# Optimization experiments

Hardware: AMD Instinct MI355X
Metric: run time of the kernel (lower is better)

## Reference

```python
import jax, jax.numpy as jnp
import numpy as np

# Adaptive softmax config (PyTorch AdaptiveLogSoftmaxWithLoss defaults, div_value=4)
N_CLASSES = 50000
CUTOFFS = (2000, 10000)          # shortlist size 2000; clusters [2000,10000), [10000,50000)
SHORTLIST = CUTOFFS[0]
HEAD_SIZE = SHORTLIST + 2        # shortlist + one logit per cluster
IN_FEAT = 512                    # output_size of MLP == in_features of adaptive softmax
HSZ0, HSZ1 = 128, 32             # in_features // 4**(i+1)
C0 = CUTOFFS[1] - CUTOFFS[0]     # 8000
C1 = N_CLASSES - CUTOFFS[1]      # 40000


def setup_inputs() -> dict:
    key = jax.random.key(0)
    ks = jax.random.split(key, 16)
    s = 0.02
    inp = {
        "x": jax.random.normal(ks[0], (4096, 512), jnp.float32),
        "t": jax.random.randint(ks[1], (4096,), 0, N_CLASSES, jnp.int64),
        # MLP params: 512 -> 2048 -> 128 -> 512, ReLU after each
        "W1": jax.random.normal(ks[2], (2048, 512), jnp.float32) * s,
        "b1": jnp.zeros((2048,), jnp.float32),
        "W2": jax.random.normal(ks[3], (128, 2048), jnp.float32) * s,
        "b2": jnp.zeros((128,), jnp.float32),
        "W3": jax.random.normal(ks[4], (512, 128), jnp.float32) * s,
        "b3": jnp.zeros((512,), jnp.float32),
        # adaptive softmax head: shortlist + 2 cluster logits
        "head_W": jax.random.normal(ks[5], (HEAD_SIZE, IN_FEAT), jnp.float32) * s,
        "head_b": jnp.zeros((HEAD_SIZE,), jnp.float32),
        # tail cluster 0: 512 -> 128 -> 8000 (no bias, no activation)
        "t0a": jax.random.normal(ks[6], (HSZ0, IN_FEAT), jnp.float32) * s,
        "t0b": jax.random.normal(ks[7], (C0, HSZ0), jnp.float32) * s,
        # tail cluster 1: 512 -> 32 -> 40000
        "t1a": jax.random.normal(ks[8], (HSZ1, IN_FEAT), jnp.float32) * s,
        "t1b": jax.random.normal(ks[9], (C1, HSZ1), jnp.float32) * s,
    }
    return inp


def _mlp(x, W1, b1, W2, b2, W3, b3):
    h = jax.nn.relu(x @ W1.T + b1)
    h = jax.nn.relu(h @ W2.T + b2)
    return jax.nn.relu(h @ W3.T + b3)   # [N, 512]


def _adaptive_log_softmax(score, t, head_W, head_b, t0a, t0b, t1a, t1b):
    n = score.shape[0]
    rows = jnp.arange(n)
    head_lsm = jax.nn.log_softmax(score @ head_W.T + head_b, axis=-1)   # [N, 2002]
    # tail clusters: two low-rank projections then log-softmax over cluster classes
    tail0_lsm = jax.nn.log_softmax((score @ t0a.T) @ t0b.T, axis=-1)    # [N, 8000]
    tail1_lsm = jax.nn.log_softmax((score @ t1a.T) @ t1b.T, axis=-1)    # [N, 40000]

    lp_short = head_lsm[rows, jnp.clip(t, 0, SHORTLIST - 1)]
    lp_c0 = head_lsm[:, SHORTLIST] + tail0_lsm[rows, jnp.clip(t - CUTOFFS[0], 0, C0 - 1)]
    lp_c1 = head_lsm[:, SHORTLIST + 1] + tail1_lsm[rows, jnp.clip(t - CUTOFFS[1], 0, C1 - 1)]

    out = jnp.where(t < CUTOFFS[0], lp_short, jnp.where(t < CUTOFFS[1], lp_c0, lp_c1))  # [N]
    loss = -jnp.mean(out)
    return out, loss


def reference(x, t, W1, b1, W2, b2, W3, b3, head_W, head_b, t0a, t0b, t1a, t1b):
    score = _mlp(x, W1, b1, W2, b2, W3, b3)
    out, loss = _adaptive_log_softmax(score, t, head_W, head_b, t0a, t0b, t1a, t1b)
    return out, loss
```

## Files before the change

### kernel.cpp

```cpp
#include <hip/hip_runtime.h>
#include <math.h>

typedef __attribute__((ext_vector_type(8))) short bf16x8;
typedef __attribute__((ext_vector_type(4))) float f32x4;

#define NROWS 4096
#define SHORTLIST 2000
#define HEADC 2002
#define CUT1 10000
#define C0_CLS 8000
#define C1_CLS 40000
#define L2E 1.4426950408889634f
#define LN2 0.6931471805599453f

#define NH_P  16
#define NC0_P 25
#define NC1_P 125

__device__ __forceinline__ float fexp2(float x) {
#if __has_builtin(__builtin_amdgcn_exp2f)
  return __builtin_amdgcn_exp2f(x);
#else
  return exp2f(x);
#endif
}

__device__ __forceinline__ unsigned short f2b(float f) {
  unsigned u = __float_as_uint(f);
  unsigned r = (u + 0x7FFFu + ((u >> 16) & 1u)) >> 16;
  return (unsigned short)r;
}
__device__ __forceinline__ float b2f(unsigned short u) {
  return __uint_as_float(((unsigned)u) << 16);
}

__device__ __forceinline__ void xcd_swz(int& bx, int& by) {
  const int gx = gridDim.x;
  const int nwg = gx * gridDim.y;
  const int orig = by * gx + bx;
  const int wg = (orig & 7) * (nwg >> 3) + (orig >> 3);
  bx = wg % gx;
  by = wg / gx;
}

__global__ __launch_bounds__(256) void cvt_all(
    const float* __restrict__ s0, unsigned short* __restrict__ d0,
    const float* __restrict__ s1, unsigned short* __restrict__ d1,
    const float* __restrict__ s2, unsigned short* __restrict__ d2,
    const float* __restrict__ s3, unsigned short* __restrict__ d3,
    const float* __restrict__ s4, unsigned short* __restrict__ d4,
    const float* __restrict__ s5, unsigned short* __restrict__ d5,
    const float* __restrict__ s6, unsigned short* __restrict__ d6,
    const float* __restrict__ s7, unsigned short* __restrict__ d7,
    const float* __restrict__ s8, unsigned short* __restrict__ d8)
{
  const float* src; unsigned short* dst; int n4;
  switch (blockIdx.y) {
    case 0: src = s0; dst = d0; n4 = 4096 * 512 / 4;   break;
    case 1: src = s1; dst = d1; n4 = 2048 * 512 / 4;   break;
    case 2: src = s2; dst = d2; n4 = 128 * 2048 / 4;   break;
    case 3: src = s3; dst = d3; n4 = 512 * 128 / 4;    break;
    case 4: src = s4; dst = d4; n4 = HEADC * 512 / 4;  break;
    case 5: src = s5; dst = d5; n4 = 128 * 512 / 4;    break;
    case 6: src = s6; dst = d6; n4 = 8000 * 128 / 4;   break;
    case 7: src = s7; dst = d7; n4 = 32 * 512 / 4;     break;
    default: src = s8; dst = d8; n4 = 40000 * 32 / 4;  break;
  }
  for (int i = blockIdx.x * 256 + threadIdx.x; i < n4; i += 256 * gridDim.x) {
    float4 v = ((const float4*)src)[i];
    ushort4 o;
    o.x = f2b(v.x); o.y = f2b(v.y); o.z = f2b(v.z); o.w = f2b(v.w);
    ((ushort4*)dst)[i] = o;
  }
}

template<bool BIAS, bool RELU, bool F32OUT, bool SCL>
__global__ __launch_bounds__(256) void gemm_lds(
    const unsigned short* __restrict__ A, const unsigned short* __restrict__ W,
    const float* __restrict__ bias, void* __restrict__ outp,
    int M, int N, int lda, int Kseg)
{
  __shared__ __align__(16) unsigned short As[128 * 32];
  __shared__ __align__(16) unsigned short Bs[128 * 32];

  int bx = blockIdx.x, by = blockIdx.y;
  xcd_swz(bx, by);

  const int tid  = threadIdx.x;
  const int lane = tid & 63;
  const int wv   = tid >> 6;
  const int cl   = lane & 15;
  const int ko   = lane >> 4;
  const int wr   = (wv >> 1) * 64;
  const int wc   = (wv & 1) * 64;
  const int row0 = by * 128;
  const int col0 = bx * 128;
  const int koff = blockIdx.z * Kseg;

  const int sr0 = tid >> 2;
  const int ssl = tid & 3;

  f32x4 acc[4][4];
#pragma unroll
  for (int p = 0; p < 4; ++p)
#pragma unroll
    for (int q = 0; q < 4; ++q) acc[p][q] = (f32x4){0.f, 0.f, 0.f, 0.f};

  const unsigned short* aSrc = A + (size_t)(row0 + sr0) * lda + koff + ssl * 8;
  const unsigned short* bSrc = W + (size_t)(col0 + sr0) * lda + koff + ssl * 8;
  const size_t half = (size_t)64 * lda;

  bf16x8 sa0 = *(const bf16x8*)(aSrc);
  bf16x8 sa1 = *(const bf16x8*)(aSrc + half);
  bf16x8 sb0 = *(const bf16x8*)(bSrc);
  bf16x8 sb1 = *(const bf16x8*)(bSrc + half);

  const int nK = Kseg / 32;
  for (int ks = 0; ks < nK; ++ks) {
    __syncthreads();
    *(bf16x8*)&As[(size_t)sr0 * 32 + ssl * 8]        = sa0;
    *(bf16x8*)&As[(size_t)(sr0 + 64) * 32 + ssl * 8] = sa1;
    *(bf16x8*)&Bs[(size_t)sr0 * 32 + ssl * 8]        = sb0;
    *(bf16x8*)&Bs[(size_t)(sr0 + 64) * 32 + ssl * 8] = sb1;
    __syncthreads();
    if (ks + 1 < nK) {
      const int k1 = (ks + 1) * 32;
      sa0 = *(const bf16x8*)(aSrc + k1);
      sa1 = *(const bf16x8*)(aSrc + k1 + half);
      sb0 = *(const bf16x8*)(bSrc + k1);
      sb1 = *(const bf16x8*)(bSrc + k1 + half);
    }
    bf16x8 aF[4], bF[4];
#pragma unroll
    for (int p = 0; p < 4; ++p)
      aF[p] = *(const bf16x8*)&As[(size_t)(wr + p * 16 + cl) * 32 + ko * 8];
#pragma unroll
    for (int q = 0; q < 4; ++q)
      bF[q] = *(const bf16x8*)&Bs[(size_t)(wc + q * 16 + cl) * 32 + ko * 8];
#pragma unroll
    for (int p = 0; p < 4; ++p)
#pragma unroll
      for (int q = 0; q < 4; ++q)
        acc[p][q] = __builtin_amdgcn_mfma_f32_16x16x32_bf16(aF[p], bF[q], acc[p][q], 0, 0, 0);
  }

  if constexpr (F32OUT) {
    float* P = (float*)outp + (size_t)blockIdx.z * M * N;
#pragma unroll
    for (int q = 0; q < 4; ++q) {
      const int col = col0 + wc + q * 16 + cl;
#pragma unroll
      for (int p = 0; p < 4; ++p)
#pragma unroll
        for (int j = 0; j < 4; ++j) {
          const int R = row0 + wr + p * 16 + 4 * ko + j;
          P[(size_t)R * N + col] = acc[p][q][j];
        }
    }
  } else {
    unsigned short* C = (unsigned short*)outp;
#pragma unroll
    for (int q = 0; q < 4; ++q) {
      const int col = col0 + wc + q * 16 + cl;
      float bs = 0.f;
      if (BIAS) bs = bias[col];
#pragma unroll
      for (int p = 0; p < 4; ++p)
#pragma unroll
        for (int j = 0; j < 4; ++j) {
          const int R = row0 + wr + p * 16 + 4 * ko + j;
          float v = acc[p][q][j] + bs;
          if (RELU) v = fmaxf(v, 0.f);
          if (SCL)  v *= L2E;
          C[(size_t)R * N + col] = f2b(v);
        }
    }
  }
}

template<int SK, bool BIAS, bool RELU>
__global__ __launch_bounds__(256) void splitk_reduce(
    const float* __restrict__ P, const float* __restrict__ bias,
    unsigned short* __restrict__ out, int MN4, int N)
{
  const int i = blockIdx.x * 256 + threadIdx.x;
  if (i >= MN4) return;
  float4 v = ((const float4*)P)[i];
#pragma unroll
  for (int z = 1; z < SK; ++z) {
    float4 p = ((const float4*)(P + (size_t)z * MN4 * 4))[i];
    v.x += p.x; v.y += p.y; v.z += p.z; v.w += p.w;
  }
  if (BIAS) {
    const int col = (i % (N / 4)) * 4;
    float4 b = *(const float4*)(bias + col);
    v.x += b.x; v.y += b.y; v.z += b.z; v.w += b.w;
  }
  if (RELU) {
    v.x = fmaxf(v.x, 0.f); v.y = fmaxf(v.y, 0.f);
    v.z = fmaxf(v.z, 0.f); v.w = fmaxf(v.w, 0.f);
  }
  ushort4 o;
  o.x = f2b(v.x); o.y = f2b(v.y); o.z = f2b(v.z); o.w = f2b(v.w);
  ((ushort4*)out)[i] = o;
}

__global__ __launch_bounds__(256) void head_gemm_lse(
    const unsigned short* __restrict__ A,
    const unsigned short* __restrict__ W,
    const float* __restrict__ bias,
    float* __restrict__ pm, float* __restrict__ ps)
{
  __shared__ __align__(16) unsigned short As[128 * 32];
  __shared__ __align__(16) unsigned short Bs[128 * 32];
  __shared__ float lm[4][64], ls[4][64];

  int bx = blockIdx.x, by = blockIdx.y;
  xcd_swz(bx, by);

  const int lda  = 512;
  const int tid  = threadIdx.x;
  const int lane = tid & 63;
  const int wv   = tid >> 6;
  const int cl   = lane & 15;
  const int ko   = lane >> 4;
  const int wr   = (wv >> 1) * 64;
  const int wc   = (wv & 1) * 64;
  const int row0 = by * 128;
  const int col0 = bx * 128;

  const int sr0 = tid >> 2;
  const int ssl = tid & 3;

  f32x4 acc[4][4];
#pragma unroll
  for (int p = 0; p < 4; ++p)
#pragma unroll
    for (int q = 0; q < 4; ++q) acc[p][q] = (f32x4){0.f, 0.f, 0.f, 0.f};

  const unsigned short* aSrc = A + (size_t)(row0 + sr0) * lda + ssl * 8;
  const unsigned short* bSrc0 = W + (size_t)min(col0 + sr0, HEADC - 1) * lda + ssl * 8;
  const unsigned short* bSrc1 = W + (size_t)min(col0 + sr0 + 64, HEADC - 1) * lda + ssl * 8;
  const size_t half = (size_t)64 * lda;

  bf16x8 sa0 = *(const bf16x8*)(aSrc);
  bf16x8 sa1 = *(const bf16x8*)(aSrc + half);
  bf16x8 sb0 = *(const bf16x8*)(bSrc0);
  bf16x8 sb1 = *(const bf16x8*)(bSrc1);

  const int nK = 512 / 32;
  for (int ks = 0; ks < nK; ++ks) {
    __syncthreads();
    *(bf16x8*)&As[(size_t)sr0 * 32 + ssl * 8]        = sa0;
    *(bf16x8*)&As[(size_t)(sr0 + 64) * 32 + ssl * 8] = sa1;
    *(bf16x8*)&Bs[(size_t)sr0 * 32 + ssl * 8]        = sb0;
    *(bf16x8*)&Bs[(size_t)(sr0 + 64) * 32 + ssl * 8] = sb1;
    __syncthreads();
    if (ks + 1 < nK) {
      const int k1 = (ks + 1) * 32;
      sa0 = *(const bf16x8*)(aSrc + k1);
      sa1 = *(const bf16x8*)(aSrc + k1 + half);
      sb0 = *(const bf16x8*)(bSrc0 + k1);
      sb1 = *(const bf16x8*)(bSrc1 + k1);
    }
    bf16x8 aF[4], bF[4];
#pragma unroll
    for (int p = 0; p < 4; ++p)
      aF[p] = *(const bf16x8*)&As[(size_t)(wr + p * 16 + cl) * 32 + ko * 8];
#pragma unroll
    for (int q = 0; q < 4; ++q)
      bF[q] = *(const bf16x8*)&Bs[(size_t)(wc + q * 16 + cl) * 32 + ko * 8];
#pragma unroll
    for (int p = 0; p < 4; ++p)
#pragma unroll
      for (int q = 0; q < 4; ++q)
        acc[p][q] = __builtin_amdgcn_mfma_f32_16x16x32_bf16(aF[p], bF[q], acc[p][q], 0, 0, 0);
  }

  float bl2[4]; int colq[4];
#pragma unroll
  for (int q = 0; q < 4; ++q) {
    colq[q] = col0 + wc + q * 16 + cl;
    bl2[q] = bias[min(colq[q], HEADC - 1)] * L2E;
  }

  float mr[4][4], sr_[4][4];
#pragma unroll
  for (int p = 0; p < 4; ++p)
#pragma unroll
    for (int j = 0; j < 4; ++j) {
      float vv[4];
#pragma unroll
      for (int q = 0; q < 4; ++q) {
        float v = acc[p][q][j] + bl2[q];
        if (colq[q] >= HEADC) v = -1e30f;
        vv[q] = v;
      }
      const float mm = fmaxf(fmaxf(vv[0], vv[1]), fmaxf(vv[2], vv[3]));
      float ss = 0.f;
#pragma unroll
      for (int q = 0; q < 4; ++q) ss += fexp2(vv[q] - mm);
      mr[p][j] = mm;
      sr_[p][j] = ss;
    }

#pragma unroll
  for (int mask = 1; mask <= 8; mask <<= 1) {
#pragma unroll
    for (int p = 0; p < 4; ++p)
#pragma unroll
      for (int j = 0; j < 4; ++j) {
        const float mo = __shfl_xor(mr[p][j], mask);
        const float so = __shfl_xor(sr_[p][j], mask);
        const float mn = fmaxf(mr[p][j], mo);
        sr_[p][j] = sr_[p][j] * fexp2(mr[p][j] - mn) + so * fexp2(mo - mn);
        mr[p][j] = mn;
      }
  }

  if (cl == 0) {
#pragma unroll
    for (int p = 0; p < 4; ++p)
#pragma unroll
      for (int j = 0; j < 4; ++j) {
        lm[wv][p * 16 + 4 * ko + j] = mr[p][j];
        ls[wv][p * 16 + 4 * ko + j] = sr_[p][j];
      }
  }
  __syncthreads();
  if (tid < 128) {
    const int pair = tid >> 6, idx = tid & 63;
    const float m0 = lm[pair * 2][idx], m1 = lm[pair * 2 + 1][idx];
    const float M = fmaxf(m0, m1);
    const float S = ls[pair * 2][idx] * fexp2(m0 - M) + ls[pair * 2 + 1][idx] * fexp2(m1 - M);
    const int grow = row0 + tid;
    pm[(size_t)bx * NROWS + grow] = M;
    ps[(size_t)bx * NROWS + grow] = S;
  }
}

template<int WR, int WC, bool BIAS, bool RELU>
__global__ __launch_bounds__(256) void gemm_mfma(
    const unsigned short* __restrict__ A, const unsigned short* __restrict__ W,
    const float* __restrict__ bias, unsigned short* __restrict__ C,
    int M, int N, int K)
{
  const int lane = threadIdx.x & 63;
  const int wv   = threadIdx.x >> 6;
  const int cl   = lane & 15;
  const int ko   = lane >> 4;
  const int rw   = (blockIdx.y * WR + (wv / WC)) * 64;
  const int cw   = (blockIdx.x * WC + (wv % WC)) * 32;

  f32x4 acc[4][2];
#pragma unroll
  for (int p = 0; p < 4; ++p)
#pragma unroll
    for (int q = 0; q < 2; ++q) acc[p][q] = (f32x4){0.f, 0.f, 0.f, 0.f};

  const unsigned short* ap = A + (size_t)(rw + cl) * K + ko * 8;
  const unsigned short* bp = W + (size_t)(cw + cl) * K + ko * 8;
  const size_t rstep = (size_t)16 * K;

#pragma unroll 2
  for (int kb = 0; kb < K; kb += 32) {
    bf16x8 a[4], b[2];
#pragma unroll
    for (int p = 0; p < 4; ++p) a[p] = *(const bf16x8*)(ap + p * rstep + kb);
#pragma unroll
    for (int q = 0; q < 2; ++q) b[q] = *(const bf16x8*)(bp + q * rstep + kb);
#pragma unroll
    for (int p = 0; p < 4; ++p)
#pragma unroll
      for (int q = 0; q < 2; ++q)
        acc[p][q] = __builtin_amdgcn_mfma_f32_16x16x32_bf16(a[p], b[q], acc[p][q], 0, 0, 0);
  }

#pragma unroll
  for (int q = 0; q < 2; ++q) {
    const int col = cw + q * 16 + cl;
    if (col >= N) continue;
    float bs = 0.f;
    if (BIAS) bs = bias[col];
#pragma unroll
    for (int p = 0; p < 4; ++p) {
#pragma unroll
      for (int j = 0; j < 4; ++j) {
        const int R = rw + p * 16 + 4 * ko + j;
        float v = acc[p][q][j] + bs;
        if (RELU) v = fmaxf(v, 0.f);
        C[(size_t)R * N + col] = f2b(v);
      }
    }
  }
}

template<int KBLK, int ROWT, int U, int NIT>
__global__ __launch_bounds__(256) void fused_lse_tail(
    const unsigned short* __restrict__ H,
    const unsigned short* __restrict__ W,
    int NCB,
    float* __restrict__ pm, float* __restrict__ ps)
{
  const int K    = KBLK * 32;
  const int lane = threadIdx.x & 63;
  const int wv   = threadIdx.x >> 6;
  const int cl   = lane & 15;
  const int ko   = lane >> 4;
  const int r0   = blockIdx.x * (64 * ROWT) + wv * (16 * ROWT);

  bf16x8 aF[ROWT][KBLK];
#pragma unroll
  for (int rt = 0; rt < ROWT; ++rt) {
    const unsigned short* ap = H + (size_t)(r0 + rt * 16 + cl) * K + ko * 8;
#pragma unroll
    for (int kk = 0; kk < KBLK; ++kk) aF[rt][kk] = *(const bf16x8*)(ap + kk * 32);
  }

  float m[ROWT][4], s[ROWT][4], s2[ROWT][4];
#pragma unroll
  for (int rt = 0; rt < ROWT; ++rt)
#pragma unroll
    for (int j = 0; j < 4; ++j) { m[rt][j] = -1e30f; s[rt][j] = 0.f; s2[rt][j] = 0.f; }

  const unsigned short* wbase =
      W + (size_t)(blockIdx.y * (U * NIT) * 16 + cl) * K + ko * 8;
  const size_t chunkstep = (size_t)16 * K;

  bf16x8 bA[U][KBLK], bB[U][KBLK];

  auto loadB = [&](bf16x8 (&bf)[U][KBLK], int it) {
    const unsigned short* p = wbase + (size_t)it * U * chunkstep;
#pragma unroll
    for (int u = 0; u < U; ++u)
#pragma unroll
      for (int kk = 0; kk < KBLK; ++kk)
        bf[u][kk] = *(const bf16x8*)(p + u * chunkstep + kk * 32);
  };

  auto consume = [&](bf16x8 (&bf)[U][KBLK]) {
    f32x4 acc[ROWT][U];
#pragma unroll
    for (int rt = 0; rt < ROWT; ++rt)
#pragma unroll
      for (int u = 0; u < U; ++u) acc[rt][u] = (f32x4){0.f, 0.f, 0.f, 0.f};
#pragma unroll
    for (int kk = 0; kk < KBLK; ++kk)
#pragma unroll
      for (int u = 0; u < U; ++u)
#pragma unroll
        for (int rt = 0; rt < ROWT; ++rt)
          acc[rt][u] = __builtin_amdgcn_mfma_f32_16x16x32_bf16(aF[rt][kk], bf[u][kk], acc[rt][u], 0, 0, 0);

    float cm[ROWT][4];
#pragma unroll
    for (int rt = 0; rt < ROWT; ++rt)
#pragma unroll
      for (int j = 0; j < 4; ++j) {
        float c = acc[rt][0][j];
#pragma unroll
        for (int u = 1; u < U; ++u) c = fmaxf(c, acc[rt][u][j]);
        cm[rt][j] = c;
      }

    float dd = -3e38f;
#pragma unroll
    for (int rt = 0; rt < ROWT; ++rt)
#pragma unroll
      for (int j = 0; j < 4; ++j) dd = fmaxf(dd, cm[rt][j] - m[rt][j]);

    if (__any(dd > 8.f)) {
#pragma unroll
      for (int rt = 0; rt < ROWT; ++rt)
#pragma unroll
        for (int j = 0; j < 4; ++j) {
          const float mn = fmaxf(m[rt][j], cm[rt][j]);
          const float sc = fexp2(m[rt][j] - mn);
          s[rt][j] *= sc; s2[rt][j] *= sc;
          m[rt][j] = mn;
        }
    }
#pragma unroll
    for (int rt = 0; rt < ROWT; ++rt)
#pragma unroll
      for (int u = 0; u < U; ++u)
#pragma unroll
        for (int j = 0; j < 4; ++j) {
          const float e = fexp2(acc[rt][u][j] - m[rt][j]);
          if (u & 1) s2[rt][j] += e; else s[rt][j] += e;
        }
  };

  loadB(bA, 0);
#pragma unroll
  for (int it = 0; it < NIT; it += 2) {
    loadB(bB, it + 1);
    consume(bA);
    if (it + 2 < NIT) loadB(bA, it + 2);
    consume(bB);
  }

#pragma unroll
  for (int rt = 0; rt < ROWT; ++rt)
#pragma unroll
    for (int j = 0; j < 4; ++j) s[rt][j] += s2[rt][j];

#pragma unroll
  for (int mask = 1; mask <= 8; mask <<= 1) {
#pragma unroll
    for (int rt = 0; rt < ROWT; ++rt)
#pragma unroll
      for (int j = 0; j < 4; ++j) {
        const float mo = __shfl_xor(m[rt][j], mask);
        const float so = __shfl_xor(s[rt][j], mask);
        const float mn = fmaxf(m[rt][j], mo);
        s[rt][j] = s[rt][j] * fexp2(m[rt][j] - mn) + so * fexp2(mo - mn);
        m[rt][j] = mn;
      }
  }
  if (cl == 0) {
#pragma unroll
    for (int rt = 0; rt < ROWT; ++rt)
#pragma unroll
      for (int j = 0; j < 4; ++j) {
        const int R = r0 + rt * 16 + 4 * ko + j;
        pm[(size_t)blockIdx.y * NROWS + R] = m[rt][j];
        ps[(size_t)blockIdx.y * NROWS + R] = s[rt][j];
      }
  }
}

__global__ __launch_bounds__(256) void gather_kernel(
    const unsigned short* __restrict__ Sb,
    const unsigned short* __restrict__ hWb,
    const float* __restrict__ head_b,
    const unsigned short* __restrict__ h0b,
    const unsigned short* __restrict__ t0bb,
    const unsigned short* __restrict__ h1b,
    const unsigned short* __restrict__ t1bb,
    const int* __restrict__ t,
    float* __restrict__ gsh, float* __restrict__ gc0, float* __restrict__ gc1,
    float* __restrict__ tg0, float* __restrict__ tg1)
{
  const int lane = threadIdx.x & 63;
  const int row  = blockIdx.x * 4 + (threadIdx.x >> 6);
  const int tv   = t[row];
  const int ch   = min(max(tv, 0), SHORTLIST - 1);
  const int c0   = min(max(tv - SHORTLIST, 0), C0_CLS - 1);
  const int c1   = min(max(tv - CUT1, 0), C1_CLS - 1);

  float acc[5] = {0.f, 0.f, 0.f, 0.f, 0.f};

  {
    bf16x8 sv = *(const bf16x8*)(Sb + (size_t)row * 512 + lane * 8);
    bf16x8 w0 = *(const bf16x8*)(hWb + (size_t)ch * 512 + lane * 8);
    bf16x8 w1 = *(const bf16x8*)(hWb + (size_t)SHORTLIST * 512 + lane * 8);
    bf16x8 w2 = *(const bf16x8*)(hWb + (size_t)(SHORTLIST + 1) * 512 + lane * 8);
#pragma unroll
    for (int e = 0; e < 8; ++e) {
      const float sf = b2f((unsigned short)sv[e]);
      acc[0] = fmaf(sf, b2f((unsigned short)w0[e]), acc[0]);
      acc[1] = fmaf(sf, b2f((unsigned short)w1[e]), acc[1]);
      acc[2] = fmaf(sf, b2f((unsigned short)w2[e]), acc[2]);
    }
  }
  if (lane < 16) {
    bf16x8 hv = *(const bf16x8*)(h0b + (size_t)row * 128 + lane * 8);
    bf16x8 wv = *(const bf16x8*)(t0bb + (size_t)c0 * 128 + lane * 8);
#pragma unroll
    for (int e = 0; e < 8; ++e)
      acc[3] = fmaf(b2f((unsigned short)hv[e]), b2f((unsigned short)wv[e]), acc[3]);
  }
  if (lane < 4) {
    bf16x8 hv = *(const bf16x8*)(h1b + (size_t)row * 32 + lane * 8);
    bf16x8 wv = *(const bf16x8*)(t1bb + (size_t)c1 * 32 + lane * 8);
#pragma unroll
    for (int e = 0; e < 8; ++e)
      acc[4] = fmaf(b2f((unsigned short)hv[e]), b2f((unsigned short)wv[e]), acc[4]);
  }

#pragma unroll
  for (int mask = 1; mask < 64; mask <<= 1)
#pragma unroll
    for (int k = 0; k < 5; ++k) acc[k] += __shfl_xor(acc[k], mask);

  if (lane == 0) {
    gsh[row] = acc[0] + head_b[ch] * L2E;
    gc0[row] = acc[1] + head_b[SHORTLIST] * L2E;
    gc1[row] = acc[2] + head_b[SHORTLIST + 1] * L2E;
    tg0[row] = acc[3];
    tg1[row] = acc[4];
  }
}

__global__ __launch_bounds__(256) void combine_kernel(
    const int* __restrict__ t,
    const float* __restrict__ pmh, const float* __restrict__ psh,
    const float* __restrict__ gsh, const float* __restrict__ gc0,
    const float* __restrict__ gc1,
    const float* __restrict__ pm0, const float* __restrict__ ps0,
    const float* __restrict__ tg0,
    const float* __restrict__ pm1, const float* __restrict__ ps1,
    const float* __restrict__ tg1,
    float* __restrict__ out)
{
  const int r = blockIdx.x * 256 + threadIdx.x;
  if (r >= NROWS) return;

  float M = -1e30f, S = 0.f;
  for (int c = 0; c < NH_P; ++c) M = fmaxf(M, pmh[c * NROWS + r]);
  for (int c = 0; c < NH_P; ++c) S += psh[c * NROWS + r] * fexp2(pmh[c * NROWS + r] - M);
  const float hl2 = M + log2f(S);

  const int tv = t[r];
  float o2;
  if (tv < SHORTLIST) {
    o2 = gsh[r] - hl2;
  } else if (tv < CUT1) {
    float M0 = -1e30f, S0 = 0.f;
    for (int c = 0; c < NC0_P; ++c) M0 = fmaxf(M0, pm0[c * NROWS + r]);
    for (int c = 0; c < NC0_P; ++c) S0 += ps0[c * NROWS + r] * fexp2(pm0[c * NROWS + r] - M0);
    o2 = (gc0[r] - hl2) + (tg0[r] - (M0 + log2f(S0)));
  } else {
    float M1 = -1e30f, S1 = 0.f;
    for (int c = 0; c < NC1_P; ++c) M1 = fmaxf(M1, pm1[c * NROWS + r]);
    for (int c = 0; c < NC1_P; ++c) S1 += ps1[c * NROWS + r] * fexp2(pm1[c * NROWS + r] - M1);
    o2 = (gc1[r] - hl2) + (tg1[r] - (M1 + log2f(S1)));
  }
  out[r] = o2 * LN2;
}

__global__ __launch_bounds__(256) void loss_kernel(
    const float* __restrict__ out, float* __restrict__ loss)
{
  __shared__ float sred[256];
  const int tid = threadIdx.x;
  float s = 0.f;
  for (int i = tid; i < NROWS; i += 256) s += out[i];
  sred[tid] = s;
  __syncthreads();
  for (int st = 128; st > 0; st >>= 1) {
    if (tid < st) sred[tid] += sred[tid + st];
    __syncthreads();
  }
  if (tid == 0) *loss = -sred[0] / (float)NROWS;
}

extern "C" void kernel_launch(void* const* d_in, const int* in_sizes, int n_in,
                              void* d_out, int out_size, void* d_ws, size_t ws_size,
                              hipStream_t stream)
{
  const float* x      = (const float*)d_in[0];
  const int*   t      = (const int*)  d_in[1];
  const float* W1     = (const float*)d_in[2];
  const float* b1     = (const float*)d_in[3];
  const float* W2     = (const float*)d_in[4];
  const float* b2     = (const float*)d_in[5];
  const float* W3     = (const float*)d_in[6];
  const float* b3     = (const float*)d_in[7];
  const float* head_W = (const float*)d_in[8];
  const float* head_b = (const float*)d_in[9];
  const float* t0a    = (const float*)d_in[10];
  const float* t0b    = (const float*)d_in[11];
  const float* t1a    = (const float*)d_in[12];
  const float* t1b    = (const float*)d_in[13];

  unsigned short* p16 = (unsigned short*)d_ws;
  unsigned short* xb  = p16; p16 += 4096ull * 512;
  unsigned short* W1b = p16; p16 += 2048ull * 512;
  unsigned short* W2b = p16; p16 += 128ull  * 2048;
  unsigned short* W3b = p16; p16 += 512ull  * 128;
  unsigned short* hWb = p16; p16 += (size_t)HEADC * 512;
  unsigned short* t0ab= p16; p16 += 128ull  * 512;
  unsigned short* t0bb= p16; p16 += 8000ull * 128;
  unsigned short* t1ab= p16; p16 += 32ull   * 512;
  unsigned short* t1bb= p16; p16 += 40000ull* 32;
  unsigned short* H1b = p16; p16 += 4096ull * 2048;
  unsigned short* H2b = p16; p16 += 4096ull * 128;
  unsigned short* Sb  = p16; p16 += 4096ull * 512;
  unsigned short* h0b = p16; p16 += 4096ull * 128;
  unsigned short* h1b = p16; p16 += 4096ull * 32;

  float* pf  = (float*)p16;
  float* pmh = pf; pf += 4096 * NH_P;
  float* psh = pf; pf += 4096 * NH_P;
  float* pm0 = pf; pf += 4096 * NC0_P;
  float* ps0 = pf; pf += 4096 * NC0_P;
  float* pm1 = pf; pf += 4096 * NC1_P;
  float* ps1 = pf; pf += 4096 * NC1_P;
  float* gsh = pf; pf += 4096;
  float* gc0 = pf; pf += 4096;
  float* gc1 = pf; pf += 4096;
  float* tg0 = pf; pf += 4096;
  float* tg1 = pf; pf += 4096;
  float* Pbuf = pf; pf += 4ull * 4096 * 128;

  float* out = (float*)d_out;

  const dim3 blk(256);

  cvt_all<<<dim3(256, 9), blk, 0, stream>>>(
      x, xb, W1, W1b, W2, W2b, W3, W3b, head_W, hWb,
      t0a, t0ab, t0b, t0bb, t1a, t1ab, t1b, t1bb);

  gemm_lds<true, true, false, false><<<dim3(16, 32), blk, 0, stream>>>(
      xb, W1b, b1, H1b, 4096, 2048, 512, 512);
  gemm_lds<false, false, true, false><<<dim3(1, 32, 4), blk, 0, stream>>>(
      H1b, W2b, nullptr, Pbuf, 4096, 128, 2048, 512);
  splitk_reduce<4, true, true><<<dim3(512), blk, 0, stream>>>(
      Pbuf, b2, H2b, 4096 * 128 / 4, 128);
  gemm_lds<true, true, false, true><<<dim3(4, 32), blk, 0, stream>>>(
      H2b, W3b, b3, Sb, 4096, 512, 128, 128);

  gemm_lds<false, false, true, false><<<dim3(1, 32, 4), blk, 0, stream>>>(
      Sb, t0ab, nullptr, Pbuf, 4096, 128, 512, 128);
  splitk_reduce<4, false, false><<<dim3(512), blk, 0, stream>>>(
      Pbuf, nullptr, h0b, 4096 * 128 / 4, 128);
  gemm_mfma<4, 1, false, false><<<dim3(1, 16), blk, 0, stream>>>(
      Sb, t1ab, nullptr, h1b, 4096, 32, 512);

  head_gemm_lse<<<dim3(16, 32), blk, 0, stream>>>(Sb, hWb, head_b, pmh, psh);

  fused_lse_tail<4, 2, 2, 10><<<dim3(32, NC0_P), blk, 0, stream>>>(h0b, t0bb, NC0_P, pm0, ps0);
  fused_lse_tail<1, 2, 5, 4 ><<<dim3(32, NC1_P), blk, 0, stream>>>(h1b, t1bb, NC1_P, pm1, ps1);

  gather_kernel<<<dim3(NROWS / 4), blk, 0, stream>>>(
      Sb, hWb, head_b, h0b, t0bb, h1b, t1bb, t, gsh, gc0, gc1, tg0, tg1);

  combine_kernel<<<dim3((NROWS + 255) / 256), blk, 0, stream>>>(
      t, pmh, psh, gsh, gc0, gc1, pm0, ps0, tg0, pm1, ps1, tg1, out);
  loss_kernel<<<dim3(1), blk, 0, stream>>>(out, out + NROWS);
}
```

Baseline: 294.5 us.

## Use direct global-to-LDS loads in GEMMs and unify tail LSE with LDS-tiled kernel

Replaces register-staged global loads plus LDS stores with direct global_load_lds transfers in the GEMM mainloops, which drops the register prefetch double-buffering and adds a trailing barrier. It also generalizes the head GEMM+logsumexp kernel to take class count, K and an optional bias. The two register-resident tail LSE kernels are replaced with this 128x128 LDS-tiled kernel, changing the partition counts to 63 and 313. The goal is to cut VGPR staging and LDS write instructions and give the tail clusters more tile reuse. In exchange it loses load/compute overlap within a block and relies on many workgroups to hide latency. For K=32 the tail-1 path runs a single iteration and pads the last column tiles.

```diff
diff --git a/kernel.cpp b/kernel.cpp
--- a/kernel.cpp
+++ b/kernel.cpp
@@ -14,8 +14,8 @@
 #define LN2 0.6931471805599453f
 
 #define NH_P  16
-#define NC0_P 25
-#define NC1_P 125
+#define NC0_P 63
+#define NC1_P 313
 
 __device__ __forceinline__ float fexp2(float x) {
 #if __has_builtin(__builtin_amdgcn_exp2f)
@@ -32,6 +32,13 @@
 }
 __device__ __forceinline__ float b2f(unsigned short u) {
   return __uint_as_float(((unsigned)u) << 16);
+}
+
+__device__ __forceinline__ void gload_lds16(const void* g, void* l) {
+  __builtin_amdgcn_global_load_lds(
+      (const __attribute__((address_space(1))) void*)g,
+      (__attribute__((address_space(3))) void*)l,
+      16, 0, 0);
 }
 
 __device__ __forceinline__ void xcd_swz(int& bx, int& by) {
@@ -110,26 +117,15 @@
   const unsigned short* bSrc = W + (size_t)(col0 + sr0) * lda + koff + ssl * 8;
   const size_t half = (size_t)64 * lda;
 
-  bf16x8 sa0 = *(const bf16x8*)(aSrc);
-  bf16x8 sa1 = *(const bf16x8*)(aSrc + half);
-  bf16x8 sb0 = *(const bf16x8*)(bSrc);
-  bf16x8 sb1 = *(const bf16x8*)(bSrc + half);
-
   const int nK = Kseg / 32;
   for (int ks = 0; ks < nK; ++ks) {
+    const int kb = ks * 32;
+    gload_lds16(aSrc + kb,        &As[tid * 8]);
+    gload_lds16(aSrc + kb + half, &As[2048 + tid * 8]);
+    gload_lds16(bSrc + kb,        &Bs[tid * 8]);
+    gload_lds16(bSrc + kb + half, &Bs[2048 + tid * 8]);
     __syncthreads();
-    *(bf16x8*)&As[(size_t)sr0 * 32 + ssl * 8]        = sa0;
-    *(bf16x8*)&As[(size_t)(sr0 + 64) * 32 + ssl * 8] = sa1;
-    *(bf16x8*)&Bs[(size_t)sr0 * 32 + ssl * 8]        = sb0;
-    *(bf16x8*)&Bs[(size_t)(sr0 + 64) * 32 + ssl * 8] = sb1;
-    __syncthreads();
-    if (ks + 1 < nK) {
-      const int k1 = (ks + 1) * 32;
-      sa0 = *(const bf16x8*)(aSrc + k1);
-      sa1 = *(const bf16x8*)(aSrc + k1 + half);
-      sb0 = *(const bf16x8*)(bSrc + k1);
-      sb1 = *(const bf16x8*)(bSrc + k1 + half);
-    }
+
     bf16x8 aF[4], bF[4];
 #pragma unroll
     for (int p = 0; p < 4; ++p)
@@ -142,6 +138,7 @@
 #pragma unroll
       for (int q = 0; q < 4; ++q)
         acc[p][q] = __builtin_amdgcn_mfma_f32_16x16x32_bf16(aF[p], bF[q], acc[p][q], 0, 0, 0);
+    __syncthreads();
   }
 
   if constexpr (F32OUT) {
@@ -205,10 +202,12 @@
   ((ushort4*)out)[i] = o;
 }
 
-__global__ __launch_bounds__(256) void head_gemm_lse(
+template<bool BIAS>
+__global__ __launch_bounds__(256) void gemm_lse(
     const unsigned short* __restrict__ A,
     const unsigned short* __restrict__ W,
     const float* __restrict__ bias,
+    int C, int lda,
     float* __restrict__ pm, float* __restrict__ ps)
 {
   __shared__ __align__(16) unsigned short As[128 * 32];
@@ -218,7 +217,6 @@
   int bx = blockIdx.x, by = blockIdx.y;
   xcd_swz(bx, by);
 
-  const int lda  = 512;
   const int tid  = threadIdx.x;
   const int lane = tid & 63;
   const int wv   = tid >> 6;
@@ -238,31 +236,20 @@
 #pragma unroll
     for (int q = 0; q < 4; ++q) acc[p][q] = (f32x4){0.f, 0.f, 0.f, 0.f};
 
-  const unsigned short* aSrc = A + (size_t)(row0 + sr0) * lda + ssl * 8;
-  const unsigned short* bSrc0 = W + (size_t)min(col0 + sr0, HEADC - 1) * lda + ssl * 8;
-  const unsigned short* bSrc1 = W + (size_t)min(col0 + sr0 + 64, HEADC - 1) * lda + ssl * 8;
+  const unsigned short* aSrc  = A + (size_t)(row0 + sr0) * lda + ssl * 8;
+  const unsigned short* bSrc0 = W + (size_t)min(col0 + sr0,      C - 1) * lda + ssl * 8;
+  const unsigned short* bSrc1 = W + (size_t)min(col0 + sr0 + 64, C - 1) * lda + ssl * 8;
   const size_t half = (size_t)64 * lda;
 
-  bf16x8 sa0 = *(const bf16x8*)(aSrc);
-  bf16x8 sa1 = *(const bf16x8*)(aSrc + half);
-  bf16x8 sb0 = *(const bf16x8*)(bSrc0);
-  bf16x8 sb1 = *(const bf16x8*)(bSrc1);
-
-  const int nK = 512 / 32;
+  const int nK = lda / 32;
   for (int ks = 0; ks < nK; ++ks) {
+    const int kb = ks * 32;
+    gload_lds16(aSrc + kb,        &As[tid * 8]);
+    gload_lds16(aSrc + kb + half, &As[2048 + tid * 8]);
+    gload_lds16(bSrc0 + kb,       &Bs[tid * 8]);
+    gload_lds16(bSrc1 + kb,       &Bs[2048 + tid * 8]);
     __syncthreads();
-    *(bf16x8*)&As[(size_t)sr0 * 32 + ssl * 8]        = sa0;
-    *(bf16x8*)&As[(size_t)(sr0 + 64) * 32 + ssl * 8] = sa1;
-    *(bf16x8*)&Bs[(size_t)sr0 * 32 + ssl * 8]        = sb0;
-    *(bf16x8*)&Bs[(size_t)(sr0 + 64) * 32 + ssl * 8] = sb1;
-    __syncthreads();
-    if (ks + 1 < nK) {
-      const int k1 = (ks + 1) * 32;
-      sa0 = *(const bf16x8*)(aSrc + k1);
-      sa1 = *(const bf16x8*)(aSrc + k1 + half);
-      sb0 = *(const bf16x8*)(bSrc0 + k1);
-      sb1 = *(const bf16x8*)(bSrc1 + k1);
-    }
+
     bf16x8 aF[4], bF[4];
 #pragma unroll
     for (int p = 0; p < 4; ++p)
@@ -275,13 +262,14 @@
 #pragma unroll
       for (int q = 0; q < 4; ++q)
         acc[p][q] = __builtin_amdgcn_mfma_f32_16x16x32_bf16(aF[p], bF[q], acc[p][q], 0, 0, 0);
+    __syncthreads();
   }
 
   float bl2[4]; int colq[4];
 #pragma unroll
   for (int q = 0; q < 4; ++q) {
     colq[q] = col0 + wc + q * 16 + cl;
-    bl2[q] = bias[min(colq[q], HEADC - 1)] * L2E;
+    bl2[q] = BIAS ? bias[min(colq[q], C - 1)] * L2E : 0.f;
   }
 
   float mr[4][4], sr_[4][4];
@@ -292,8 +280,8 @@
       float vv[4];
 #pragma unroll
       for (int q = 0; q < 4; ++q) {
-        float v = acc[p][q][j] + bl2[q];
-        if (colq[q] >= HEADC) v = -1e30f;
+        float v = BIAS ? (acc[p][q][j] + bl2[q]) : acc[p][q][j];
+        if (colq[q] >= C) v = -1e30f;
         vv[q] = v;
       }
       const float mm = fmaxf(fmaxf(vv[0], vv[1]), fmaxf(vv[2], vv[3]));
@@ -392,141 +380,6 @@
         C[(size_t)R * N + col] = f2b(v);
       }
     }
-  }
-}
-
-template<int KBLK, int ROWT, int U, int NIT>
-__global__ __launch_bounds__(256) void fused_lse_tail(
-    const unsigned short* __restrict__ H,
-    const unsigned short* __restrict__ W,
-    int NCB,
-    float* __restrict__ pm, float* __restrict__ ps)
-{
-  const int K    = KBLK * 32;
-  const int lane = threadIdx.x & 63;
-  const int wv   = threadIdx.x >> 6;
-  const int cl   = lane & 15;
-  const int ko   = lane >> 4;
-  const int r0   = blockIdx.x * (64 * ROWT) + wv * (16 * ROWT);
-
-  bf16x8 aF[ROWT][KBLK];
-#pragma unroll
-  for (int rt = 0; rt < ROWT; ++rt) {
-    const unsigned short* ap = H + (size_t)(r0 + rt * 16 + cl) * K + ko * 8;
-#pragma unroll
-    for (int kk = 0; kk < KBLK; ++kk) aF[rt][kk] = *(const bf16x8*)(ap + kk * 32);
-  }
-
-  float m[ROWT][4], s[ROWT][4], s2[ROWT][4];
-#pragma unroll
-  for (int rt = 0; rt < ROWT; ++rt)
-#pragma unroll
-    for (int j = 0; j < 4; ++j) { m[rt][j] = -1e30f; s[rt][j] = 0.f; s2[rt][j] = 0.f; }
-
-  const unsigned short* wbase =
-      W + (size_t)(blockIdx.y * (U * NIT) * 16 + cl) * K + ko * 8;
-  const size_t chunkstep = (size_t)16 * K;
-
-  bf16x8 bA[U][KBLK], bB[U][KBLK];
-
-  auto loadB = [&](bf16x8 (&bf)[U][KBLK], int it) {
-    const unsigned short* p = wbase + (size_t)it * U * chunkstep;
-#pragma unroll
-    for (int u = 0; u < U; ++u)
-#pragma unroll
-      for (int kk = 0; kk < KBLK; ++kk)
-        bf[u][kk] = *(const bf16x8*)(p + u * chunkstep + kk * 32);
-  };
-
-  auto consume = [&](bf16x8 (&bf)[U][KBLK]) {
-    f32x4 acc[ROWT][U];
-#pragma unroll
-    for (int rt = 0; rt < ROWT; ++rt)
-#pragma unroll
-      for (int u = 0; u < U; ++u) acc[rt][u] = (f32x4){0.f, 0.f, 0.f, 0.f};
-#pragma unroll
-    for (int kk = 0; kk < KBLK; ++kk)
-#pragma unroll
-      for (int u = 0; u < U; ++u)
-#pragma unroll
-        for (int rt = 0; rt < ROWT; ++rt)
-          acc[rt][u] = __builtin_amdgcn_mfma_f32_16x16x32_bf16(aF[rt][kk], bf[u][kk], acc[rt][u], 0, 0, 0);
-
-    float cm[ROWT][4];
-#pragma unroll
-    for (int rt = 0; rt < ROWT; ++rt)
-#pragma unroll
-      for (int j = 0; j < 4; ++j) {
-        float c = acc[rt][0][j];
-#pragma unroll
-        for (int u = 1; u < U; ++u) c = fmaxf(c, acc[rt][u][j]);
-        cm[rt][j] = c;
-      }
-
-    float dd = -3e38f;
-#pragma unroll
-    for (int rt = 0; rt < ROWT; ++rt)
-#pragma unroll
-      for (int j = 0; j < 4; ++j) dd = fmaxf(dd, cm[rt][j] - m[rt][j]);
-
-    if (__any(dd > 8.f)) {
-#pragma unroll
-      for (int rt = 0; rt < ROWT; ++rt)
-#pragma unroll
-        for (int j = 0; j < 4; ++j) {
-          const float mn = fmaxf(m[rt][j], cm[rt][j]);
-          const float sc = fexp2(m[rt][j] - mn);
-          s[rt][j] *= sc; s2[rt][j] *= sc;
-          m[rt][j] = mn;
-        }
-    }
-#pragma unroll
-    for (int rt = 0; rt < ROWT; ++rt)
-#pragma unroll
-      for (int u = 0; u < U; ++u)
-#pragma unroll
-        for (int j = 0; j < 4; ++j) {
-          const float e = fexp2(acc[rt][u][j] - m[rt][j]);
-          if (u & 1) s2[rt][j] += e; else s[rt][j] += e;
-        }
-  };
-
-  loadB(bA, 0);
-#pragma unroll
-  for (int it = 0; it < NIT; it += 2) {
-    loadB(bB, it + 1);
-    consume(bA);
-    if (it + 2 < NIT) loadB(bA, it + 2);
-    consume(bB);
-  }
-
-#pragma unroll
-  for (int rt = 0; rt < ROWT; ++rt)
-#pragma unroll
-    for (int j = 0; j < 4; ++j) s[rt][j] += s2[rt][j];
-
-#pragma unroll
-  for (int mask = 1; mask <= 8; mask <<= 1) {
-#pragma unroll
-    for (int rt = 0; rt < ROWT; ++rt)
-#pragma unroll
-      for (int j = 0; j < 4; ++j) {
-        const float mo = __shfl_xor(m[rt][j], mask);
-        const float so = __shfl_xor(s[rt][j], mask);
-        const float mn = fmaxf(m[rt][j], mo);
-        s[rt][j] = s[rt][j] * fexp2(m[rt][j] - mn) + so * fexp2(mo - mn);
-        m[rt][j] = mn;
-      }
-  }
-  if (cl == 0) {
-#pragma unroll
-    for (int rt = 0; rt < ROWT; ++rt)
-#pragma unroll
-      for (int j = 0; j < 4; ++j) {
-        const int R = r0 + rt * 16 + 4 * ko + j;
-        pm[(size_t)blockIdx.y * NROWS + R] = m[rt][j];
-        ps[(size_t)blockIdx.y * NROWS + R] = s[rt][j];
-      }
   }
 }
 
@@ -719,10 +572,9 @@
   gemm_mfma<4, 1, false, false><<<dim3(1, 16), blk, 0, stream>>>(
       Sb, t1ab, nullptr, h1b, 4096, 32, 512);
 
-  head_gemm_lse<<<dim3(16, 32), blk, 0, stream>>>(Sb, hWb, head_b, pmh, psh);
-
-  fused_lse_tail<4, 2, 2, 10><<<dim3(32, NC0_P), blk, 0, stream>>>(h0b, t0bb, NC0_P, pm0, ps0);
-  fused_lse_tail<1, 2, 5, 4 ><<<dim3(32, NC1_P), blk, 0, stream>>>(h1b, t1bb, NC1_P, pm1, ps1);
+  gemm_lse<true ><<<dim3(NH_P,  32), blk, 0, stream>>>(Sb,  hWb,  head_b, HEADC,  512, pmh, psh);
+  gemm_lse<false><<<dim3(NC0_P, 32), blk, 0, stream>>>(h0b, t0bb, nullptr, C0_CLS, 128, pm0, ps0);
+  gemm_lse<false><<<dim3(NC1_P, 32), blk, 0, stream>>>(h1b, t1bb, nullptr, C1_CLS, 32,  pm1, ps1);
 
   gather_kernel<<<dim3(NROWS / 4), blk, 0, stream>>>(
       Sb, hWb, head_b, h0b, t0bb, h1b, t1bb, t, gsh, gc0, gc1, tg0, tg1);
```

After: 411.0 us. 1.4x slower.
